# Kernel optimization log

Hardware: AMD Instinct MI355X
Metric: run time of the kernel (lower is better)

Reference implementation:

```python
import jax, jax.numpy as jnp
import numpy as np

NUM_HEADS = 8
GROUPS = 32
EPS = 1e-5


def group_norm(x, gamma, beta):
    # x: (b, c, L)
    b, c, L = x.shape
    xg = x.reshape(b, GROUPS, c // GROUPS, L)
    mean = xg.mean(axis=(2, 3), keepdims=True)
    var = xg.var(axis=(2, 3), keepdims=True)
    xn = ((xg - mean) / jnp.sqrt(var + EPS)).reshape(b, c, L)
    return xn * gamma[None, :, None] + beta[None, :, None]


def setup_inputs() -> dict:
    key = jax.random.key(0)
    ks = jax.random.split(key, 8)
    b, c, h, w = 8, 512, 32, 32
    inner = c  # inner_channels == -1 -> channels
    x = jax.random.normal(ks[0], (b, c, h, w), dtype=jnp.float32)
    gamma = jnp.ones((c,), dtype=jnp.float32)
    beta = jnp.zeros((c,), dtype=jnp.float32)
    Wq = jax.random.normal(ks[1], (inner, c), dtype=jnp.float32) * 0.02
    bq = jnp.zeros((inner,), dtype=jnp.float32)
    Wkv = jax.random.normal(ks[2], (2 * inner, c), dtype=jnp.float32) * 0.02
    bkv = jnp.zeros((2 * inner,), dtype=jnp.float32)
    Wo = jax.random.normal(ks[3], (c, inner), dtype=jnp.float32) * 0.02
    bo = jnp.zeros((c,), dtype=jnp.float32)
    return {"x": x, "gamma": gamma, "beta": beta, "Wq": Wq, "bq": bq,
            "Wkv": Wkv, "bkv": bkv, "Wo": Wo, "bo": bo}


def reference(x, gamma, beta, Wq, bq, Wkv, bkv, Wo, bo):
    b, c = x.shape[:2]
    spatial = x.shape[2:]
    L = int(np.prod(spatial))
    inner = Wq.shape[0]
    dh = inner // NUM_HEADS
    scale = dh ** -0.5  # NOTE: applied to BOTH q and k, as in the source

    xr = x.reshape(b, c, L)
    hn = group_norm(xr, gamma, beta)          # norm(x); also serves as context

    # 1x1 Conv1d == channel matmul
    q = jnp.einsum('oc,bcl->bol', Wq, hn) + bq[None, :, None]
    kv = jnp.einsum('oc,bcl->bol', Wkv, hn) + bkv[None, :, None]
    k, v = jnp.split(kv, 2, axis=1)

    # (b, heads, dh, L)
    qh = (q * scale).reshape(b, NUM_HEADS, dh, L)
    kh = (k * scale).reshape(b, NUM_HEADS, dh, L)
    vh = v.reshape(b, NUM_HEADS, dh, L)

    dots = jnp.einsum('bhdt,bhds->bhts', qh, kh)
    attn = jax.nn.softmax(dots.astype(jnp.float32), axis=-1).astype(dots.dtype)
    out = jnp.einsum('bhts,bhds->bhdt', attn, vh)  # (b, heads, dh, L)

    out = out.reshape(b, inner, L)
    # output Linear over the channel dim
    out = jnp.einsum('oc,bcl->bol', Wo, out) + bo[None, :, None]
    return (xr + out).reshape(b, c, *spatial)
```

## Files before the change

### kernel.cpp

```cpp
#include <hip/hip_runtime.h>
#include <math.h>

#define B_ 8
#define C_ 512
#define L_ 1024
#define NH_ 8
#define DH_ 64
#define EPS 1e-5f
#define SCALE 0.125f
#define QSCALE (0.125f * 1.44269504088896f)

typedef __bf16 bf16x8 __attribute__((ext_vector_type(8)));
typedef __bf16 bf16x4 __attribute__((ext_vector_type(4)));
typedef float  f32x4  __attribute__((ext_vector_type(4)));

#define MFMA16(a, b, c) __builtin_amdgcn_mfma_f32_16x16x32_bf16((a), (b), (c), 0, 0, 0)

__device__ __forceinline__ void glds16(const __bf16* g, __bf16* l) {
    __builtin_amdgcn_global_load_lds((const __attribute__((address_space(1))) void*)(g),
                                     (__attribute__((address_space(3))) void*)(l),
                                     16, 0, 0);
}

__global__ __launch_bounds__(256)
void prep_kernel(const float* __restrict__ Wq, const float* __restrict__ Wkv,
                 const float* __restrict__ Wo, __bf16* __restrict__ dst,
                 const float* __restrict__ x, float* __restrict__ stats) {
    __shared__ float rs[256], rss[256];
    int bid = blockIdx.x, tid = threadIdx.x;
    if (bid < 1024) {
        int idx = bid * 256 + tid;
        float4 v;
        if (idx < 65536)        v = ((const float4*)Wq)[idx];
        else if (idx < 196608)  v = ((const float4*)Wkv)[idx - 65536];
        else                    v = ((const float4*)Wo)[idx - 196608];
        bf16x4 o;
        o[0] = (__bf16)v.x; o[1] = (__bf16)v.y; o[2] = (__bf16)v.z; o[3] = (__bf16)v.w;
        ((bf16x4*)dst)[idx] = o;
        return;
    }
    int bg = bid - 1024;
    size_t goff = (size_t)bg * 16 * L_;
    const float4* x4 = (const float4*)(x + goff);
    float s = 0.f, ss = 0.f;
    for (int i = tid; i < 4096; i += 256) {
        float4 v = x4[i];
        s  += v.x + v.y + v.z + v.w;
        ss += v.x * v.x + v.y * v.y + v.z * v.z + v.w * v.w;
    }
    rs[tid] = s; rss[tid] = ss;
    __syncthreads();
    for (int off = 128; off > 0; off >>= 1) {
        if (tid < off) { rs[tid] += rs[tid + off]; rss[tid] += rss[tid + off]; }
        __syncthreads();
    }
    if (tid == 0) {
        const float inv_n = 1.f / 16384.f;
        float mean = rs[0] * inv_n;
        float var  = rss[0] * inv_n - mean * mean;
        stats[bg * 2]     = mean;
        stats[bg * 2 + 1] = rsqrtf(var + EPS);
    }
}

__global__ __launch_bounds__(256)
void gn_apply_kernel(const float* __restrict__ x, const float* __restrict__ gamma,
                     const float* __restrict__ beta, const float* __restrict__ stats,
                     __bf16* __restrict__ hnT) {
    __shared__ __bf16 T[32 * 520];
    const int lt = blockIdx.x, b = blockIdx.y;
    const int tid = threadIdx.x;
    const int l0 = lt * 32;
    const int cbase = tid >> 3, fl = tid & 7;
#pragma unroll
    for (int p = 0; p < 16; ++p) {
        int cc = cbase + p * 32;
        float4 v = *(const float4*)&x[((size_t)b * C_ + cc) * L_ + l0 + fl * 4];
        int bg = b * 32 + (cc >> 4);
        float m = stats[bg * 2], rstd = stats[bg * 2 + 1];
        float ga = gamma[cc] * rstd, be = beta[cc];
        T[(fl * 4 + 0) * 520 + cc] = (__bf16)((v.x - m) * ga + be);
        T[(fl * 4 + 1) * 520 + cc] = (__bf16)((v.y - m) * ga + be);
        T[(fl * 4 + 2) * 520 + cc] = (__bf16)((v.z - m) * ga + be);
        T[(fl * 4 + 3) * 520 + cc] = (__bf16)((v.w - m) * ga + be);
    }
    __syncthreads();
    const int lrow = tid >> 6, cu = tid & 63;
#pragma unroll
    for (int pp = 0; pp < 8; ++pp) {
        int l = pp * 4 + lrow;
        bf16x8 r = *(const bf16x8*)&T[l * 520 + cu * 8];
        *(bf16x8*)&hnT[((size_t)b * L_ + l0 + l) * C_ + cu * 8] = r;
    }
}

__device__ __forceinline__
void gemm_mainloop(const __bf16* __restrict__ A, const __bf16* __restrict__ Bp,
                   __bf16* As, __bf16* Bs, f32x4 acc[4][4]) {
    const int tid = threadIdx.x;
    const int lane = tid & 63, w = tid >> 6;
    const int c = lane & 15, q = lane >> 4;
    const int wm = (w >> 1) * 64, wn = (w & 1) * 64;
    const int l8 = lane >> 3, kgsw = (lane & 7) ^ l8;

    for (int k0 = 0; k0 < 512; k0 += 64) {
#pragma unroll
        for (int i = 0; i < 4; ++i) {
            int chunk = w * 4 + i;
            int row = chunk * 8 + l8;
            glds16(A  + (size_t)row * 512 + k0 + kgsw * 8, &As[chunk * 512]);
            glds16(Bp + (size_t)row * 512 + k0 + kgsw * 8, &Bs[chunk * 512]);
        }
        __syncthreads();
#pragma unroll
        for (int ks = 0; ks < 2; ++ks) {
            const int koff = ((ks * 4 + q) ^ (c & 7)) * 8;
            bf16x8 af[4], bfr[4];
#pragma unroll
            for (int m = 0; m < 4; ++m)
                af[m] = *(const bf16x8*)&As[(wm + m * 16 + c) * 64 + koff];
#pragma unroll
            for (int n = 0; n < 4; ++n)
                bfr[n] = *(const bf16x8*)&Bs[(wn + n * 16 + c) * 64 + koff];
#pragma unroll
            for (int m = 0; m < 4; ++m)
#pragma unroll
                for (int n = 0; n < 4; ++n)
                    acc[m][n] = MFMA16(af[m], bfr[n], acc[m][n]);
        }
        __syncthreads();
    }
}

__global__ __launch_bounds__(256)
void qkv_kernel(const __bf16* __restrict__ Wq_bf, const __bf16* __restrict__ Wkv_bf,
                const __bf16* __restrict__ hnT,
                const float* __restrict__ bq, const float* __restrict__ bkv,
                __bf16* __restrict__ qT, __bf16* __restrict__ kT,
                __bf16* __restrict__ vv) {
    __shared__ __bf16 SMEM[128 * 64 * 2];
    __bf16* As = SMEM;
    __bf16* Bs = SMEM + 128 * 64;
    const int b = blockIdx.y;
    const int xx = blockIdx.x;
    const int wt = xx % 12, oi = xx / 12;
    const int sec = wt >> 2;
    const __bf16* hb = hnT + (size_t)b * L_ * C_;

    const __bf16 *A, *Bp;
    int m0, n0;
    if (sec < 2) {
        m0 = (wt & 3) * 128; n0 = oi * 128;
        A  = (sec == 0 ? Wq_bf : Wkv_bf) + (size_t)m0 * 512;
        Bp = hb + (size_t)n0 * 512;
    } else {
        m0 = oi * 128; n0 = (wt & 3) * 128;
        A  = hb + (size_t)m0 * 512;
        Bp = Wkv_bf + (size_t)(512 + n0) * 512;
    }

    f32x4 acc[4][4];
#pragma unroll
    for (int m = 0; m < 4; ++m)
#pragma unroll
        for (int n = 0; n < 4; ++n)
#pragma unroll
            for (int r = 0; r < 4; ++r) acc[m][n][r] = 0.f;

    gemm_mainloop(A, Bp, As, Bs, acc);

    const int tid = threadIdx.x, lane = tid & 63, w = tid >> 6;
    const int c = lane & 15, q = lane >> 4;
    const int wm = (w >> 1) * 64, wn = (w & 1) * 64;

    __bf16* T2 = SMEM;
    const float* bias = (sec == 0) ? bq : bkv;
    const float scl = (sec == 0) ? QSCALE : SCALE;
#pragma unroll
    for (int mt = 0; mt < 4; ++mt)
#pragma unroll
        for (int nt = 0; nt < 4; ++nt) {
            int n_loc = wn + nt * 16 + c;
            int u4 = (wm >> 2) + mt * 4 + q;
            int u4sw = u4 ^ ((n_loc & 7) << 1);
            bf16x4 ov;
            if (sec < 2) {
                int ob = m0 + wm + mt * 16 + q * 4;
#pragma unroll
                for (int r = 0; r < 4; ++r)
                    ov[r] = (__bf16)((acc[mt][nt][r] + bias[ob + r]) * scl);
            } else {
                float bi = bkv[512 + n0 + n_loc];
#pragma unroll
                for (int r = 0; r < 4; ++r)
                    ov[r] = (__bf16)(acc[mt][nt][r] + bi);
            }
            *(bf16x4*)&T2[n_loc * 128 + u4sw * 4] = ov;
        }
    __syncthreads();
#pragma unroll
    for (int p = 0; p < 8; ++p) {
        int rrow = p * 16 + (tid >> 4);
        int u16 = tid & 15;
        int u4p = (u16 * 2) ^ ((rrow & 7) << 1);
        bf16x8 val = *(const bf16x8*)&T2[rrow * 128 + u4p * 4];
        if (sec < 2) {
            int l = n0 + rrow;
            int og = m0 + u16 * 8;
            int hh = og >> 6, d0 = og & 63;
            __bf16* dstp = (sec == 0) ? qT : kT;
            *(bf16x8*)&dstp[((size_t)(b * NH_ + hh) * L_ + l) * DH_ + d0] = val;
        } else {
            int o = n0 + rrow;
            int lg = m0 + u16 * 8;
            *(bf16x8*)&vv[((size_t)b * C_ + o) * L_ + lg] = val;
        }
    }
}

__global__ __launch_bounds__(256)
void attn_kernel(const __bf16* __restrict__ qT, const __bf16* __restrict__ kT,
                 const __bf16* __restrict__ vv, __bf16* __restrict__ aoT) {
    const int tt = blockIdx.x, h = blockIdx.y, b = blockIdx.z;
    const int t0 = tt * 64;
    __shared__ __bf16 Ks[64 * 64];
    __shared__ __bf16 Vs[64 * 64];
    __shared__ __bf16 Ps[64 * 72];

    const int tid = threadIdx.x, lane = tid & 63, w = tid >> 6;
    const int c = lane & 15, q = lane >> 4;
    const int l8 = lane >> 3, kg = (lane & 7) ^ l8;

    const __bf16* qbase = qT + ((size_t)(b * NH_ + h) * L_ + t0) * DH_;
    const __bf16* kbase = kT + (size_t)(b * NH_ + h) * L_ * DH_;
    const __bf16* vbase = vv + (size_t)(b * C_ + h * DH_) * L_;

    bf16x8 bQ[2];
#pragma unroll
    for (int ks = 0; ks < 2; ++ks)
        bQ[ks] = *(const bf16x8*)&qbase[(size_t)(w * 16 + c) * DH_ + ks * 32 + q * 8];

    bf16x8 aO;
#pragma unroll
    for (int j = 0; j < 8; ++j) aO[j] = (c == 0) ? (__bf16)1.0f : (__bf16)0.0f;

    f32x4 o_acc[4], o_l;
#pragma unroll
    for (int dt = 0; dt < 4; ++dt)
#pragma unroll
        for (int r = 0; r < 4; ++r) o_acc[dt][r] = 0.f;
#pragma unroll
    for (int r = 0; r < 4; ++r) o_l[r] = 0.f;

    for (int s0 = 0; s0 < L_; s0 += 64) {
#pragma unroll
        for (int i = 0; i < 2; ++i) {
            int chunk = w * 2 + i;
            int row = chunk * 8 + l8;
            glds16(kbase + (size_t)(s0 + row) * DH_ + kg * 8, &Ks[chunk * 512]);
            glds16(vbase + (size_t)row * L_ + s0 + kg * 8, &Vs[chunk * 512]);
        }
        __syncthreads();

        f32x4 sres[4];
#pragma unroll
        for (int mt = 0; mt < 4; ++mt)
#pragma unroll
            for (int r = 0; r < 4; ++r) sres[mt][r] = 0.f;
#pragma unroll
        for (int ks = 0; ks < 2; ++ks) {
            const int koff = ((ks * 4 + q) ^ (c & 7)) * 8;
#pragma unroll
            for (int mt = 0; mt < 4; ++mt) {
                bf16x8 aK = *(const bf16x8*)&Ks[(mt * 16 + c) * 64 + koff];
                sres[mt] = MFMA16(aK, bQ[ks], sres[mt]);
            }
        }

#pragma unroll
        for (int mt = 0; mt < 4; ++mt) {
            bf16x4 pv;
#pragma unroll
            for (int r = 0; r < 4; ++r) pv[r] = (__bf16)exp2f(sres[mt][r]);
            *(bf16x4*)&Ps[(w * 16 + c) * 72 + (mt * 4 + q) * 4] = pv;
        }

#pragma unroll
        for (int ks = 0; ks < 2; ++ks) {
            const int koff = ((ks * 4 + q) ^ (c & 7)) * 8;
            bf16x8 bp = *(const bf16x8*)&Ps[(w * 16 + c) * 72 + ks * 32 + q * 8];
#pragma unroll
            for (int dt = 0; dt < 4; ++dt) {
                bf16x8 aV = *(const bf16x8*)&Vs[(dt * 16 + c) * 64 + koff];
                o_acc[dt] = MFMA16(aV, bp, o_acc[dt]);
            }
            o_l = MFMA16(aO, bp, o_l);
        }
        __syncthreads();
    }

    float lsum = __shfl(o_l[0], c);
    float linv = 1.f / lsum;
    int tg = t0 + w * 16 + c;
    __bf16* aobase = aoT + ((size_t)b * L_ + tg) * C_ + h * DH_;
#pragma unroll
    for (int dt = 0; dt < 4; ++dt) {
        bf16x4 ov;
#pragma unroll
        for (int r = 0; r < 4; ++r) ov[r] = (__bf16)(o_acc[dt][r] * linv);
        *(bf16x4*)&aobase[dt * 16 + q * 4] = ov;
    }
}

__global__ __launch_bounds__(256)
void proj_kernel(const __bf16* __restrict__ aoT, const __bf16* __restrict__ Wo_bf,
                 const float* __restrict__ bo, const float* __restrict__ x,
                 float* __restrict__ out) {
    __shared__ __bf16 As[128 * 64], Bs[128 * 64];
    const int b = blockIdx.y, t = blockIdx.x;
    const int m0 = (t >> 2) * 128;
    const int n0 = (t & 3) * 128;
    const __bf16* A  = aoT + (size_t)b * L_ * C_ + (size_t)m0 * 512;
    const __bf16* Bp = Wo_bf + (size_t)n0 * 512;

    f32x4 acc[4][4];
#pragma unroll
    for (int m = 0; m < 4; ++m)
#pragma unroll
        for (int n = 0; n < 4; ++n)
#pragma unroll
            for (int r = 0; r < 4; ++r) acc[m][n][r] = 0.f;

    gemm_mainloop(A, Bp, As, Bs, acc);

    const int tid = threadIdx.x, lane = tid & 63, w = tid >> 6;
    const int c = lane & 15, q = lane >> 4;
    const int wm = (w >> 1) * 64, wn = (w & 1) * 64;

#pragma unroll
    for (int mt = 0; mt < 4; ++mt)
#pragma unroll
        for (int nt = 0; nt < 4; ++nt) {
            int lb = m0 + wm + mt * 16 + q * 4;
            int o  = n0 + wn + nt * 16 + c;
            float bi = bo[o];
            size_t off = ((size_t)b * C_ + o) * L_ + lb;
            float4 xv = *(const float4*)&x[off];
            float4 rv;
            rv.x = acc[mt][nt][0] + bi + xv.x;
            rv.y = acc[mt][nt][1] + bi + xv.y;
            rv.z = acc[mt][nt][2] + bi + xv.z;
            rv.w = acc[mt][nt][3] + bi + xv.w;
            *(float4*)&out[off] = rv;
        }
}

extern "C" void kernel_launch(void* const* d_in, const int* in_sizes, int n_in,
                              void* d_out, int out_size, void* d_ws, size_t ws_size,
                              hipStream_t stream) {
    const float* x     = (const float*)d_in[0];
    const float* gamma = (const float*)d_in[1];
    const float* beta  = (const float*)d_in[2];
    const float* Wq    = (const float*)d_in[3];
    const float* bq    = (const float*)d_in[4];
    const float* Wkv   = (const float*)d_in[5];
    const float* bkv   = (const float*)d_in[6];
    const float* Wo    = (const float*)d_in[7];
    const float* bo    = (const float*)d_in[8];
    float* out = (float*)d_out;

    __bf16* wsb = (__bf16*)d_ws;
    __bf16* Wq_bf  = wsb;
    __bf16* Wkv_bf = wsb + 262144;
    __bf16* Wo_bf  = wsb + 786432;
    __bf16* hnT    = wsb + 1048576;
    __bf16* qT     = wsb + 5242880;
    __bf16* kT     = wsb + 9437184;
    __bf16* vv     = wsb + 13631488;
    __bf16* aoT    = wsb + 17825792;
    float*  stats  = (float*)(wsb + 22020096);

    prep_kernel<<<dim3(1280), 256, 0, stream>>>(Wq, Wkv, Wo, wsb, x, stats);
    gn_apply_kernel<<<dim3(32, B_), 256, 0, stream>>>(x, gamma, beta, stats, hnT);
    qkv_kernel<<<dim3(96, B_), 256, 0, stream>>>(Wq_bf, Wkv_bf, hnT, bq, bkv, qT, kT, vv);
    attn_kernel<<<dim3(16, NH_, B_), 256, 0, stream>>>(qT, kT, vv, aoT);
    proj_kernel<<<dim3(32, B_), 256, 0, stream>>>(aoT, Wo_bf, bo, x, out);
}
```

Measured before the change: 173.5 us.

## Use per-wave private LDS staging in GEMM mainloop to remove block barriers

Rewrites the shared GEMM mainloop so each wave loads only its own 64-row A and B slices into a private LDS region with a K-step of 32. This replaces the per-iteration __syncthreads with a vmcnt wait. Adds launch_bounds occupancy hints and a barrier before the epilogue reuses LDS. In exchange, A and B tiles are now loaded redundantly by the waves that share them, which doubles global/L2 traffic. The smaller K-step also means more loop iterations with less latency hiding.

```diff
diff --git a/kernel.cpp b/kernel.cpp
--- a/kernel.cpp
+++ b/kernel.cpp
@@ -95,52 +95,47 @@
 }
 
 __device__ __forceinline__
-void gemm_mainloop(const __bf16* __restrict__ A, const __bf16* __restrict__ Bp,
-                   __bf16* As, __bf16* Bs, f32x4 acc[4][4]) {
+void gemm_mainloop_wp(const __bf16* __restrict__ A, const __bf16* __restrict__ Bp,
+                      __bf16* SMEM, f32x4 acc[4][4]) {
     const int tid = threadIdx.x;
     const int lane = tid & 63, w = tid >> 6;
     const int c = lane & 15, q = lane >> 4;
     const int wm = (w >> 1) * 64, wn = (w & 1) * 64;
-    const int l8 = lane >> 3, kgsw = (lane & 7) ^ l8;
-
-    for (int k0 = 0; k0 < 512; k0 += 64) {
+    const int r16 = lane >> 2;
+    const int kp  = (lane & 3) * 8;
+
+    __bf16* Aw = SMEM + w * 4096;
+    __bf16* Bw = Aw + 2048;
+
+    for (int k0 = 0; k0 < 512; k0 += 32) {
 #pragma unroll
         for (int i = 0; i < 4; ++i) {
-            int chunk = w * 4 + i;
-            int row = chunk * 8 + l8;
-            glds16(A  + (size_t)row * 512 + k0 + kgsw * 8, &As[chunk * 512]);
-            glds16(Bp + (size_t)row * 512 + k0 + kgsw * 8, &Bs[chunk * 512]);
-        }
-        __syncthreads();
-#pragma unroll
-        for (int ks = 0; ks < 2; ++ks) {
-            const int koff = ((ks * 4 + q) ^ (c & 7)) * 8;
-            bf16x8 af[4], bfr[4];
-#pragma unroll
-            for (int m = 0; m < 4; ++m)
-                af[m] = *(const bf16x8*)&As[(wm + m * 16 + c) * 64 + koff];
+            glds16(A  + (size_t)(wm + i * 16 + r16) * 512 + k0 + kp, Aw + i * 512);
+            glds16(Bp + (size_t)(wn + i * 16 + r16) * 512 + k0 + kp, Bw + i * 512);
+        }
+        __builtin_amdgcn_s_waitcnt(0x0F70);
+        bf16x8 af[4], bfr[4];
+#pragma unroll
+        for (int m = 0; m < 4; ++m)
+            af[m] = *(const bf16x8*)&Aw[(m * 16 + c) * 32 + q * 8];
+#pragma unroll
+        for (int n = 0; n < 4; ++n)
+            bfr[n] = *(const bf16x8*)&Bw[(n * 16 + c) * 32 + q * 8];
+#pragma unroll
+        for (int m = 0; m < 4; ++m)
 #pragma unroll
             for (int n = 0; n < 4; ++n)
-                bfr[n] = *(const bf16x8*)&Bs[(wn + n * 16 + c) * 64 + koff];
-#pragma unroll
-            for (int m = 0; m < 4; ++m)
-#pragma unroll
-                for (int n = 0; n < 4; ++n)
-                    acc[m][n] = MFMA16(af[m], bfr[n], acc[m][n]);
-        }
-        __syncthreads();
-    }
-}
-
-__global__ __launch_bounds__(256)
+                acc[m][n] = MFMA16(af[m], bfr[n], acc[m][n]);
+    }
+}
+
+__global__ __launch_bounds__(256, 3)
 void qkv_kernel(const __bf16* __restrict__ Wq_bf, const __bf16* __restrict__ Wkv_bf,
                 const __bf16* __restrict__ hnT,
                 const float* __restrict__ bq, const float* __restrict__ bkv,
                 __bf16* __restrict__ qT, __bf16* __restrict__ kT,
                 __bf16* __restrict__ vv) {
-    __shared__ __bf16 SMEM[128 * 64 * 2];
-    __bf16* As = SMEM;
-    __bf16* Bs = SMEM + 128 * 64;
+    __shared__ __bf16 SMEM[16384];
     const int b = blockIdx.y;
     const int xx = blockIdx.x;
     const int wt = xx % 12, oi = xx / 12;
@@ -167,12 +162,13 @@
 #pragma unroll
             for (int r = 0; r < 4; ++r) acc[m][n][r] = 0.f;
 
-    gemm_mainloop(A, Bp, As, Bs, acc);
+    gemm_mainloop_wp(A, Bp, SMEM, acc);
 
     const int tid = threadIdx.x, lane = tid & 63, w = tid >> 6;
     const int c = lane & 15, q = lane >> 4;
     const int wm = (w >> 1) * 64, wn = (w & 1) * 64;
 
+    __syncthreads();
     __bf16* T2 = SMEM;
     const float* bias = (sec == 0) ? bq : bkv;
     const float scl = (sec == 0) ? QSCALE : SCALE;
@@ -312,11 +308,11 @@
     }
 }
 
-__global__ __launch_bounds__(256)
+__global__ __launch_bounds__(256, 3)
 void proj_kernel(const __bf16* __restrict__ aoT, const __bf16* __restrict__ Wo_bf,
                  const float* __restrict__ bo, const float* __restrict__ x,
                  float* __restrict__ out) {
-    __shared__ __bf16 As[128 * 64], Bs[128 * 64];
+    __shared__ __bf16 SMEM[16384];
     const int b = blockIdx.y, t = blockIdx.x;
     const int m0 = (t >> 2) * 128;
     const int n0 = (t & 3) * 128;
@@ -331,7 +327,7 @@
 #pragma unroll
             for (int r = 0; r < 4; ++r) acc[m][n][r] = 0.f;
 
-    gemm_mainloop(A, Bp, As, Bs, acc);
+    gemm_mainloop_wp(A, Bp, SMEM, acc);
 
     const int tid = threadIdx.x, lane = tid & 63, w = tid >> 6;
     const int c = lane & 15, q = lane >> 4;
```

Result: no change. 176.8 us (+1.9%).

## Switch attention to 32x32x16 MFMA with 128-query tiles per block

Applied to the files above, without the earlier changes.

Reworks the attention kernel so each wave handles 32 query rows using 32x32x16 bf16 MFMAs instead of 16x16x32, doubling the query tile per block to 128 and halving the grid. Each K/V tile loaded into LDS is reused across twice as many queries, which cuts global/LDS traffic per unit of work, and the larger MFMA shape lowers instruction count. The P staging buffer becomes per-wave with an XOR swizzle. The cost is fewer blocks (512) for occupancy and more accumulator registers per thread.

```diff
diff --git a/kernel.cpp b/kernel.cpp
--- a/kernel.cpp
+++ b/kernel.cpp
@@ -13,8 +13,10 @@
 typedef __bf16 bf16x8 __attribute__((ext_vector_type(8)));
 typedef __bf16 bf16x4 __attribute__((ext_vector_type(4)));
 typedef float  f32x4  __attribute__((ext_vector_type(4)));
+typedef float  f32x16 __attribute__((ext_vector_type(16)));
 
 #define MFMA16(a, b, c) __builtin_amdgcn_mfma_f32_16x16x32_bf16((a), (b), (c), 0, 0, 0)
+#define MFMA32(a, b, c) __builtin_amdgcn_mfma_f32_32x32x16_bf16((a), (b), (c), 0, 0, 0)
 
 __device__ __forceinline__ void glds16(const __bf16* g, __bf16* l) {
     __builtin_amdgcn_global_load_lds((const __attribute__((address_space(1))) void*)(g),
@@ -222,94 +224,96 @@
 void attn_kernel(const __bf16* __restrict__ qT, const __bf16* __restrict__ kT,
                  const __bf16* __restrict__ vv, __bf16* __restrict__ aoT) {
     const int tt = blockIdx.x, h = blockIdx.y, b = blockIdx.z;
-    const int t0 = tt * 64;
+    const int t0 = tt * 128;
     __shared__ __bf16 Ks[64 * 64];
     __shared__ __bf16 Vs[64 * 64];
-    __shared__ __bf16 Ps[64 * 72];
+    __shared__ __bf16 Ps[4 * 32 * 64];
 
     const int tid = threadIdx.x, lane = tid & 63, w = tid >> 6;
-    const int c = lane & 15, q = lane >> 4;
+    const int tc = lane & 31, half = lane >> 5;
     const int l8 = lane >> 3, kg = (lane & 7) ^ l8;
+    const int t7 = tc & 7;
 
     const __bf16* qbase = qT + ((size_t)(b * NH_ + h) * L_ + t0) * DH_;
     const __bf16* kbase = kT + (size_t)(b * NH_ + h) * L_ * DH_;
     const __bf16* vbase = vv + (size_t)(b * C_ + h * DH_) * L_;
-
-    bf16x8 bQ[2];
-#pragma unroll
-    for (int ks = 0; ks < 2; ++ks)
-        bQ[ks] = *(const bf16x8*)&qbase[(size_t)(w * 16 + c) * DH_ + ks * 32 + q * 8];
+    __bf16* Pw = &Ps[w * 2048];
+
+    bf16x8 bQ[4];
+#pragma unroll
+    for (int kc = 0; kc < 4; ++kc)
+        bQ[kc] = *(const bf16x8*)&qbase[(size_t)(w * 32 + tc) * DH_ + kc * 16 + half * 8];
 
     bf16x8 aO;
 #pragma unroll
-    for (int j = 0; j < 8; ++j) aO[j] = (c == 0) ? (__bf16)1.0f : (__bf16)0.0f;
-
-    f32x4 o_acc[4], o_l;
-#pragma unroll
-    for (int dt = 0; dt < 4; ++dt)
-#pragma unroll
-        for (int r = 0; r < 4; ++r) o_acc[dt][r] = 0.f;
-#pragma unroll
-    for (int r = 0; r < 4; ++r) o_l[r] = 0.f;
+    for (int j = 0; j < 8; ++j) aO[j] = (tc == 0) ? (__bf16)1.0f : (__bf16)0.0f;
+
+    f32x16 o_acc[2], o_l;
+#pragma unroll
+    for (int r = 0; r < 16; ++r) { o_acc[0][r] = 0.f; o_acc[1][r] = 0.f; o_l[r] = 0.f; }
 
     for (int s0 = 0; s0 < L_; s0 += 64) {
 #pragma unroll
-        for (int i = 0; i < 2; ++i) {
-            int chunk = w * 2 + i;
-            int row = chunk * 8 + l8;
-            glds16(kbase + (size_t)(s0 + row) * DH_ + kg * 8, &Ks[chunk * 512]);
-            glds16(vbase + (size_t)row * L_ + s0 + kg * 8, &Vs[chunk * 512]);
-        }
-        __syncthreads();
-
-        f32x4 sres[4];
-#pragma unroll
-        for (int mt = 0; mt < 4; ++mt)
-#pragma unroll
-            for (int r = 0; r < 4; ++r) sres[mt][r] = 0.f;
-#pragma unroll
-        for (int ks = 0; ks < 2; ++ks) {
-            const int koff = ((ks * 4 + q) ^ (c & 7)) * 8;
-#pragma unroll
-            for (int mt = 0; mt < 4; ++mt) {
-                bf16x8 aK = *(const bf16x8*)&Ks[(mt * 16 + c) * 64 + koff];
-                sres[mt] = MFMA16(aK, bQ[ks], sres[mt]);
+        for (int ci = 0; ci < 2; ++ci) {
+            int chunkrow = ci * 32 + w * 8;
+            glds16(kbase + (size_t)(s0 + chunkrow + l8) * DH_ + kg * 8,
+                   &Ks[chunkrow * 64]);
+            glds16(vbase + (size_t)(chunkrow + l8) * L_ + s0 + kg * 8,
+                   &Vs[chunkrow * 64]);
+        }
+        __syncthreads();
+
+        f32x16 sres[2];
+#pragma unroll
+        for (int r = 0; r < 16; ++r) { sres[0][r] = 0.f; sres[1][r] = 0.f; }
+#pragma unroll
+        for (int kc = 0; kc < 4; ++kc) {
+            const int koff = ((kc * 2 + half) ^ t7) * 8;
+#pragma unroll
+            for (int sh = 0; sh < 2; ++sh) {
+                bf16x8 aK = *(const bf16x8*)&Ks[(sh * 32 + tc) * 64 + koff];
+                sres[sh] = MFMA32(aK, bQ[kc], sres[sh]);
             }
         }
 
 #pragma unroll
-        for (int mt = 0; mt < 4; ++mt) {
-            bf16x4 pv;
-#pragma unroll
-            for (int r = 0; r < 4; ++r) pv[r] = (__bf16)exp2f(sres[mt][r]);
-            *(bf16x4*)&Ps[(w * 16 + c) * 72 + (mt * 4 + q) * 4] = pv;
-        }
-
-#pragma unroll
-        for (int ks = 0; ks < 2; ++ks) {
-            const int koff = ((ks * 4 + q) ^ (c & 7)) * 8;
-            bf16x8 bp = *(const bf16x8*)&Ps[(w * 16 + c) * 72 + ks * 32 + q * 8];
-#pragma unroll
-            for (int dt = 0; dt < 4; ++dt) {
-                bf16x8 aV = *(const bf16x8*)&Vs[(dt * 16 + c) * 64 + koff];
-                o_acc[dt] = MFMA16(aV, bp, o_acc[dt]);
+        for (int sh = 0; sh < 2; ++sh)
+#pragma unroll
+            for (int rq = 0; rq < 4; ++rq) {
+                bf16x4 pv;
+#pragma unroll
+                for (int r = 0; r < 4; ++r) pv[r] = (__bf16)exp2f(sres[sh][rq * 4 + r]);
+                *(bf16x4*)&Pw[tc * 64 + ((sh * 4 + rq) ^ t7) * 8 + half * 4] = pv;
             }
-            o_l = MFMA16(aO, bp, o_l);
-        }
-        __syncthreads();
-    }
-
-    float lsum = __shfl(o_l[0], c);
+
+#pragma unroll
+        for (int kc = 0; kc < 4; ++kc) {
+            const int koff = ((kc * 2 + half) ^ t7) * 8;
+            bf16x8 bp = *(const bf16x8*)&Pw[tc * 64 + koff];
+#pragma unroll
+            for (int dh = 0; dh < 2; ++dh) {
+                bf16x8 aV = *(const bf16x8*)&Vs[(dh * 32 + tc) * 64 + koff];
+                o_acc[dh] = MFMA32(aV, bp, o_acc[dh]);
+            }
+            o_l = MFMA32(aO, bp, o_l);
+        }
+        __syncthreads();
+    }
+
+    float lsum = __shfl(o_l[0], tc);
     float linv = 1.f / lsum;
-    int tg = t0 + w * 16 + c;
+    int tg = t0 + w * 32 + tc;
     __bf16* aobase = aoT + ((size_t)b * L_ + tg) * C_ + h * DH_;
 #pragma unroll
-    for (int dt = 0; dt < 4; ++dt) {
-        bf16x4 ov;
-#pragma unroll
-        for (int r = 0; r < 4; ++r) ov[r] = (__bf16)(o_acc[dt][r] * linv);
-        *(bf16x4*)&aobase[dt * 16 + q * 4] = ov;
-    }
+    for (int dh = 0; dh < 2; ++dh)
+#pragma unroll
+        for (int rq = 0; rq < 4; ++rq) {
+            int d0 = dh * 32 + rq * 8 + half * 4;
+            bf16x4 ov;
+#pragma unroll
+            for (int r = 0; r < 4; ++r) ov[r] = (__bf16)(o_acc[dh][rq * 4 + r] * linv);
+            *(bf16x4*)&aobase[d0] = ov;
+        }
 }
 
 __global__ __launch_bounds__(256)
@@ -383,6 +387,6 @@
     prep_kernel<<<dim3(1280), 256, 0, stream>>>(Wq, Wkv, Wo, wsb, x, stats);
     gn_apply_kernel<<<dim3(32, B_), 256, 0, stream>>>(x, gamma, beta, stats, hnT);
     qkv_kernel<<<dim3(96, B_), 256, 0, stream>>>(Wq_bf, Wkv_bf, hnT, bq, bkv, qT, kT, vv);
-    attn_kernel<<<dim3(16, NH_, B_), 256, 0, stream>>>(qT, kT, vv, aoT);
+    attn_kernel<<<dim3(8, NH_, B_), 256, 0, stream>>>(qT, kT, vv, aoT);
     proj_kernel<<<dim3(32, B_), 256, 0, stream>>>(aoT, Wo_bf, bo, x, out);
 }
```

New measurement: 174.1 us. Within noise of the previous version (+0.3%).
